# Kernel optimization log

Measured on AMD Instinct MI355X. Metric: run time of the kernel, lower is better.

The kernel has to match this reference:

```python
import jax, jax.numpy as jnp
import numpy as np

GRID = 104          # grid cells per side (832px input, stride 8)
NB = 9              # anchors per cell
NC = 80             # classes
INPUT_SIZE = 832    # draw canvas size
DET_T = 0.02        # detection threshold
NMS_T = 0.3         # IoU threshold
MAX_BOXES = 50      # per-class NMS cap
N = GRID * GRID * NB


def setup_inputs() -> dict:
    key = jax.random.key(0)
    k1, k2 = jax.random.split(key)
    inputs = jax.random.normal(k1, (1, GRID, GRID, NB, 5 + NC), dtype=jnp.float32)
    anchors = jax.random.uniform(k2, (NB, 2), dtype=jnp.float32, minval=0.5, maxval=GRID / 2.0)
    return {"inputs": inputs, "anchors": anchors}


def _iou_one_vs_all(box, boxes):
    # box [4], boxes [N,4]; coordinate order is irrelevant to IoU as long as consistent
    x1 = jnp.maximum(box[0], boxes[:, 0]); y1 = jnp.maximum(box[1], boxes[:, 1])
    x2 = jnp.minimum(box[2], boxes[:, 2]); y2 = jnp.minimum(box[3], boxes[:, 3])
    inter = jnp.maximum(x2 - x1, 0.0) * jnp.maximum(y2 - y1, 0.0)
    a0 = (box[2] - box[0]) * (box[3] - box[1])
    a1 = (boxes[:, 2] - boxes[:, 0]) * (boxes[:, 3] - boxes[:, 1])
    union = a0 + a1 - inter
    return jnp.where(union > 0, inter / union, 0.0)


def _forward(inputs, anchors):
    # ---- decode boxes ----
    gy, gx = jnp.meshgrid(jnp.arange(GRID), jnp.arange(GRID), indexing='ij')
    c_grid = jnp.stack([gx, gy], axis=-1).astype(inputs.dtype)[None, :, :, None, :]  # (1,G,G,1,2)
    b_xy = (jax.nn.sigmoid(inputs[..., 0:2]) + c_grid) / GRID
    b_wh = jnp.exp(inputs[..., 2:4]) * anchors[None, None, None, :, :] / GRID
    boxes = jnp.concatenate([b_xy - b_wh / 2.0, b_xy + b_wh / 2.0], axis=-1)
    scores_all = jax.nn.sigmoid(inputs[..., 4:5]) * jax.nn.softmax(inputs[..., 5:], axis=-1)
    scores_all = scores_all * (scores_all > DET_T).astype(scores_all.dtype)
    classes = jnp.argmax(scores_all, axis=-1)
    scores = jnp.max(scores_all, axis=-1)

    fboxes = boxes.reshape(N, 4)
    fscores = scores.reshape(N)
    fclasses = classes.reshape(N)

    # ---- per-class masked scores [NC, N] ----
    cls_mask = (fclasses[None, :] == jnp.arange(NC)[:, None]) & (fscores[None, :] > 0)
    cls_scores = jnp.where(cls_mask, fscores[None, :], 0.0)

    # ---- greedy NMS, vmapped over classes ----
    def nms_one(s):
        def body(i, carry):
            s, inds, valid = carry
            idx = jnp.argmax(s)
            v = s[idx] > 0
            ious = _iou_one_vs_all(fboxes[idx], fboxes)
            s = jnp.where(ious > NMS_T, 0.0, s).at[idx].set(0.0)
            return s, inds.at[i].set(idx), valid.at[i].set(v)
        init = (s, jnp.zeros(MAX_BOXES, jnp.int32), jnp.zeros(MAX_BOXES, dtype=bool))
        _, inds, valid = jax.lax.fori_loop(0, MAX_BOXES, body, init)
        return inds, valid

    inds, valid = jax.vmap(nms_one)(cls_scores)  # [NC, MAX_BOXES]
    sel = inds.reshape(-1)
    val = valid.reshape(-1)
    sboxes = fboxes[sel]  # [NC*MAX_BOXES, 4]; TF interprets as (y1, x1, y2, x2)

    # ---- draw bounding boxes on (1,H,W,1) canvas ----
    H = W = INPUT_SIZE
    def to_px(v, size):
        return jnp.clip(jnp.round(v * (size - 1)), 0, size - 1).astype(jnp.int32)
    r1 = to_px(sboxes[:, 0], H); c1 = to_px(sboxes[:, 1], W)
    r2 = to_px(sboxes[:, 2], H); c2 = to_px(sboxes[:, 3], W)
    cols = jnp.arange(W); rows = jnp.arange(H)
    col_in = ((cols[None, :] >= c1[:, None]) & (cols[None, :] <= c2[:, None]) & val[:, None]).astype(jnp.float32)
    row_in = ((rows[None, :] >= r1[:, None]) & (rows[None, :] <= r2[:, None]) & val[:, None]).astype(jnp.float32)
    canvas = jnp.zeros((H, W), jnp.float32)
    canvas = canvas.at[r1].add(col_in).at[r2].add(col_in)          # horizontal edges
    canvas = (canvas.T.at[c1].add(row_in).at[c2].add(row_in)).T   # vertical edges
    return (canvas > 0).astype(jnp.float32)[None, :, :, None]


def reference(inputs, anchors):
    return _forward(inputs, anchors)
```

## Files before the change

### kernel.cpp

```cpp
#pragma clang fp contract(off)
#include <hip/hip_runtime.h>
#include <math.h>

#define G       104
#define NBA     9
#define NC      80
#define NBOX    (G*G*NBA)
#define CH      (5+NC)
#define DET_T_  0.02f
#define NMS_T_  0.3f
#define MAXB    50
#define SORTN   2048
#define IMG     832
#define DB      128

typedef unsigned long long u64;
typedef unsigned int       u32;

__device__ __forceinline__ float sigmoidf_(float x) { return 1.0f / (1.0f + expf(-x)); }

__global__ __launch_bounds__(DB) void decode_kernel(const float* __restrict__ in,
        const float* __restrict__ anchors,
        float4* __restrict__ boxById, u64* __restrict__ allKey, float4* __restrict__ out4)
{
    __shared__ float lds[DB * CH];
    const int tid = threadIdx.x;

    {
        const int CZ = (IMG*IMG/4 + 760) / 761;
        int zbase = blockIdx.x * CZ;
        for (int i = tid; i < CZ; i += DB) {
            int idx = zbase + i;
            if (idx < IMG*IMG/4) out4[idx] = make_float4(0, 0, 0, 0);
        }
    }

    const int base = blockIdx.x * (DB * CH);
    int nfl = NBOX * CH - base;
    if (nfl > DB * CH) nfl = DB * CH;

    int nv4 = nfl >> 2;
    const float4* gin4 = (const float4*)(in + base);
    for (int i = tid; i < nv4; i += DB) ((float4*)lds)[i] = gin4[i];
    for (int i = (nv4 << 2) + tid; i < nfl; i += DB) lds[i] = in[base + i];
    __syncthreads();

    int n = blockIdx.x * DB + tid;
    if (n >= NBOX) return;
    const float* p = lds + tid * CH;

    float v[CH];
#pragma unroll
    for (int k = 0; k < CH; ++k) v[k] = p[k];

    float m = v[5];
#pragma unroll
    for (int i = 1; i < NC; ++i) m = fmaxf(m, v[5 + i]);

    float sum = 0.0f;
    u64 cm0 = 0, cm1 = 0;
#pragma unroll
    for (int i = 0; i < NC; ++i) {
        float d = v[5 + i] - m;
        sum += expf(d);
        u64 cand = (d >= -2.0e-6f) ? 1ull : 0ull;
        if (i < 64) cm0 |= cand << i;
        else        cm1 |= cand << (i - 64);
    }
    float obj = sigmoidf_(v[4]);

    float best = -1.0f; int bcls = 0;
    while (cm0) {
        int i = __ffsll((long long)cm0) - 1; cm0 &= cm0 - 1;
        float e = expf(p[5 + i] - m);
        float s = obj * (e / sum);
        if (s > best) { best = s; bcls = i; }
    }
    while (cm1) {
        int i = __ffsll((long long)cm1) - 1 + 64; cm1 &= cm1 - 1;
        float e = expf(p[5 + i] - m);
        float s = obj * (e / sum);
        if (s > best) { best = s; bcls = i; }
    }

    u64 key = 0;
    if (best > DET_T_) {
        int a  = n % NBA;
        int t2 = n / NBA;
        int gx = t2 % G;
        int gy = t2 / G;
        float bx = (sigmoidf_(v[0]) + (float)gx) / (float)G;
        float by = (sigmoidf_(v[1]) + (float)gy) / (float)G;
        float bw = expf(v[2]) * anchors[2*a + 0] / (float)G;
        float bh = expf(v[3]) * anchors[2*a + 1] / (float)G;
        boxById[n] = make_float4(bx - bw / 2.0f, by - bh / 2.0f,
                                 bx + bw / 2.0f, by + bh / 2.0f);
        key = ((u64)__float_as_uint(best) << 24) | ((u64)(131071 - n) << 7) | (u64)bcls;
    }
    allKey[n] = key;
}

__device__ __forceinline__ int to_px(float v) {
    float r = rintf(v * 831.0f);
    r = fminf(fmaxf(r, 0.0f), 831.0f);
    return (int)r;
}

__device__ __forceinline__ bool iou_gt_pre(const float4 W, float aW,
                                           const float4 C, float aC) {
    float x1 = fmaxf(W.x, C.x), y1 = fmaxf(W.y, C.y);
    float x2 = fminf(W.z, C.z), y2 = fminf(W.w, C.w);
    float inter = fmaxf(x2 - x1, 0.0f) * fmaxf(y2 - y1, 0.0f);
    float uni = aW + aC - inter;
    float iou = (uni > 0.0f) ? (inter / uni) : 0.0f;
    return iou > NMS_T_;
}

__device__ __forceinline__ u64 cex_shfl(u64 r, int x, int stride, int size) {
    u64 v = __shfl_xor(r, stride);
    bool asc   = (x & size) != 0;
    bool upper = (x & stride) != 0;
    bool keep_max = (!asc) != upper;
    u64 mx = (r > v) ? r : v;
    u64 mn = (r > v) ? v : r;
    return keep_max ? mx : mn;
}

__global__ __launch_bounds__(1024) void nms_draw_kernel(
    const float4* __restrict__ boxById, const u64* __restrict__ allKey,
    float* __restrict__ out)
{
    __shared__ u64    skey[SORTN];
    __shared__ float4 sbox[SORTN];
    __shared__ float4 selb[MAXB];
    __shared__ float  swa[MAXB];
    __shared__ u64    csA[16], csB[16], sfirst[16];
    __shared__ int    s_nsel, s_bad, s_cnt;

    const int c = blockIdx.x;
    const int t = threadIdx.x;
    const int w = t >> 6, l = t & 63;
    const int eA = (w << 7) + l, eB = eA + 64;

    if (t == 0) { s_bad = 0; s_nsel = 0; s_cnt = 0; }
    for (int i = t; i < SORTN; i += 1024) skey[i] = 0;
    __syncthreads();

    {
        const ulonglong2* ak2 = (const ulonglong2*)allKey;
        for (int pi = t; pi < NBOX/2; pi += 1024) {
            ulonglong2 kk = ak2[pi];
            if (kk.x != 0ull && (int)(kk.x & 0x7F) == c) {
                int pos = atomicAdd(&s_cnt, 1);
                if (pos < SORTN) skey[pos] = kk.x;
            }
            if (kk.y != 0ull && (int)(kk.y & 0x7F) == c) {
                int pos = atomicAdd(&s_cnt, 1);
                if (pos < SORTN) skey[pos] = kk.y;
            }
        }
    }
    __syncthreads();
    int count = s_cnt; if (count > SORTN) count = SORTN;

    u64 rA = skey[eA];
    u64 rB = skey[eB];

    {
        u64 x = rA ^ rB;
#pragma unroll
        for (int off = 32; off >= 1; off >>= 1) x ^= __shfl_xor(x, off);
        if (l == 0) csA[w] = x;
    }

#pragma unroll
    for (int size = 2; size <= 64; size <<= 1)
        for (int stride = size >> 1; stride >= 1; stride >>= 1) {
            rA = cex_shfl(rA, eA, stride, size);
            rB = cex_shfl(rB, eB, stride, size);
        }
    {
        const int size = 128;
        bool asc = (eA & 128) != 0;
        u64 mx = (rA > rB) ? rA : rB, mn = (rA > rB) ? rB : rA;
        rA = asc ? mn : mx; rB = asc ? mx : mn;
        for (int stride = 32; stride >= 1; stride >>= 1) {
            rA = cex_shfl(rA, eA, stride, size);
            rB = cex_shfl(rB, eB, stride, size);
        }
    }

    for (int size = 256; size <= 2048; size <<= 1) {
        skey[eA] = rA; skey[eB] = rB;
        __syncthreads();
        for (int stride = size >> 1; stride >= 128; stride >>= 1) {
            int i = ((t & ~(stride - 1)) << 1) | (t & (stride - 1));
            int j = i | stride;
            bool asc = (i & size) != 0;
            u64 ki = skey[i], kj = skey[j];
            bool sw = asc ? (ki > kj) : (ki < kj);
            if (sw) { skey[i] = kj; skey[j] = ki; }
            __syncthreads();
        }
        rA = skey[eA]; rB = skey[eB];
        bool asc = (eA & size) != 0;
        u64 mx = (rA > rB) ? rA : rB, mn = (rA > rB) ? rB : rA;
        rA = asc ? mn : mx; rB = asc ? mx : mn;
        for (int stride = 32; stride >= 1; stride >>= 1) {
            rA = cex_shfl(rA, eA, stride, size);
            rB = cex_shfl(rB, eB, stride, size);
        }
    }

    {
        u64 x = rA ^ rB;
#pragma unroll
        for (int off = 32; off >= 1; off >>= 1) x ^= __shfl_xor(x, off);
        if (l == 0) { csB[w] = x; sfirst[w] = rA; }
        bool bad = false;
        u64 dA  = __shfl_down(rA, 1);
        u64 dB  = __shfl_down(rB, 1);
        u64 rB0 = __shfl(rB, 0);
        if (l < 63) { bad |= (rA < dA); bad |= (rB < dB); }
        if (l == 63) bad |= (rA < rB0);
        __syncthreads();
        if (l == 63 && w < 15) bad |= (rB < sfirst[w + 1]);
        if (t == 0) {
            u64 X0 = 0, X1 = 0;
            for (int i = 0; i < 16; ++i) { X0 ^= csA[i]; X1 ^= csB[i]; }
            if (X0 != X1) s_bad = 1;
        }
        if (bad) s_bad = 1;
        __syncthreads();
    }

    if (s_bad) {
        for (int i = t; i < SORTN; i += 1024) skey[i] = 0;
        if (t == 0) s_cnt = 0;
        __syncthreads();
        for (int i = t; i < NBOX; i += 1024) {
            u64 k = allKey[i];
            if (k != 0ull && (int)(k & 0x7F) == c) {
                int pos = atomicAdd(&s_cnt, 1);
                if (pos < SORTN) skey[pos] = k;
            }
        }
        __syncthreads();
        for (int ph = 0; ph < SORTN; ++ph) {
            int i = (t << 1) + (ph & 1);
            if (i + 1 < SORTN) {
                u64 a = skey[i], b = skey[i + 1];
                if (a < b) { skey[i] = b; skey[i + 1] = a; }
            }
            __syncthreads();
        }
        rA = skey[eA]; rB = skey[eB];
    }

    if (eA < count) sbox[eA] = boxById[131071 - (int)((rA >> 7) & 0x1FFFF)];
    if (eB < count) sbox[eB] = boxById[131071 - (int)((rB >> 7) & 0x1FFFF)];
    __syncthreads();

    if (t < 64) {
        const int lane = t;
        int nsel = 0;
        for (int p0 = 0; p0 < count && nsel < MAXB; p0 += 64) {
            int p = p0 + lane;
            bool have = (p < count);
            float4 C = sbox[have ? p : 0];
            float aC = (C.z - C.x) * (C.w - C.y);

            bool sup = false;
#pragma unroll 4
            for (int ww = 0; ww < nsel; ++ww)
                sup |= iou_gt_pre(selb[ww], swa[ww], C, aC);

            u64 alive = __ballot(have && !sup);
            while (alive != 0ull && nsel < MAXB) {
                int i = __ffsll((long long)alive) - 1;
                float4 Wn = make_float4(__shfl(C.x, i), __shfl(C.y, i),
                                        __shfl(C.z, i), __shfl(C.w, i));
                float aWn = __shfl(aC, i);
                if (lane == 0) { selb[nsel] = Wn; swa[nsel] = aWn; }
                ++nsel;
                u64 killed = __ballot(have && iou_gt_pre(Wn, aWn, C, aC));
                alive &= ~killed;
            }
        }
        if (lane == 0) s_nsel = nsel;
    }
    __syncthreads();

    int nsel = s_nsel;
    int lane = t & 63;
    for (int b = t >> 6; b < nsel; b += 16) {
        float4 B = selb[b];
        int r1 = to_px(B.x), c1 = to_px(B.y), r2 = to_px(B.z), c2 = to_px(B.w);
        for (int i = c1 + lane; i <= c2; i += 64) {
            out[r1*IMG + i] = 1.0f;
            out[r2*IMG + i] = 1.0f;
        }
        for (int i = r1 + lane; i <= r2; i += 64) {
            out[i*IMG + c1] = 1.0f;
            out[i*IMG + c2] = 1.0f;
        }
    }
}

extern "C" void kernel_launch(void* const* d_in, const int* in_sizes, int n_in,
                              void* d_out, int out_size, void* d_ws, size_t ws_size,
                              hipStream_t stream)
{
    const float* in      = (const float*)d_in[0];
    const float* anchors = (const float*)d_in[1];
    float* out           = (float*)d_out;

    char* ws = (char*)d_ws;
    float4* boxById = (float4*)ws;
    u64*    allKey  = (u64*)(ws + (size_t)NBOX * sizeof(float4));

    decode_kernel<<<(NBOX + DB - 1)/DB, DB, 0, stream>>>(in, anchors, boxById, allKey,
                                                         (float4*)out);
    nms_draw_kernel<<<NC, 1024, 0, stream>>>(boxById, allKey, out);
}
```

Before: 79.70 us.

## Split drawing into row-tiled kernel with LDS canvas instead of scattered global writes

Removes the canvas zeroing from the decode kernel and the scattered global stores from the NMS kernel. NMS now writes the selected boxes as pixel coordinates to a workspace buffer. A new draw kernel gives each block 8 image rows, rasterises every selected box into an LDS row buffer with a run queue for horizontal edges, and writes the rows out coalesced. This trades one extra kernel launch and a full scan of all 4000 box slots per block for no separate zero pass and no uncoalesced global writes.

```diff
diff --git a/kernel.cpp b/kernel.cpp
--- a/kernel.cpp
+++ b/kernel.cpp
@@ -10,9 +10,13 @@
 #define DET_T_  0.02f
 #define NMS_T_  0.3f
 #define MAXB    50
+#define NSEL    (NC*MAXB)
 #define SORTN   2048
 #define IMG     832
 #define DB      128
+#define RPB     8
+#define DCHUNK  1024
+#define RQCAP   (2*DCHUNK)
 
 typedef unsigned long long u64;
 typedef unsigned int       u32;
@@ -21,19 +25,10 @@
 
 __global__ __launch_bounds__(DB) void decode_kernel(const float* __restrict__ in,
         const float* __restrict__ anchors,
-        float4* __restrict__ boxById, u64* __restrict__ allKey, float4* __restrict__ out4)
+        float4* __restrict__ boxById, u64* __restrict__ allKey)
 {
     __shared__ float lds[DB * CH];
     const int tid = threadIdx.x;
-
-    {
-        const int CZ = (IMG*IMG/4 + 760) / 761;
-        int zbase = blockIdx.x * CZ;
-        for (int i = tid; i < CZ; i += DB) {
-            int idx = zbase + i;
-            if (idx < IMG*IMG/4) out4[idx] = make_float4(0, 0, 0, 0);
-        }
-    }
 
     const int base = blockIdx.x * (DB * CH);
     int nfl = NBOX * CH - base;
@@ -126,9 +121,9 @@
     return keep_max ? mx : mn;
 }
 
-__global__ __launch_bounds__(1024) void nms_draw_kernel(
+__global__ __launch_bounds__(1024) void nms_select_kernel(
     const float4* __restrict__ boxById, const u64* __restrict__ allKey,
-    float* __restrict__ out)
+    ushort4* __restrict__ selPx)
 {
     __shared__ u64    skey[SORTN];
     __shared__ float4 sbox[SORTN];
@@ -292,19 +287,67 @@
     __syncthreads();
 
     int nsel = s_nsel;
-    int lane = t & 63;
-    for (int b = t >> 6; b < nsel; b += 16) {
-        float4 B = selb[b];
-        int r1 = to_px(B.x), c1 = to_px(B.y), r2 = to_px(B.z), c2 = to_px(B.w);
-        for (int i = c1 + lane; i <= c2; i += 64) {
-            out[r1*IMG + i] = 1.0f;
-            out[r2*IMG + i] = 1.0f;
-        }
-        for (int i = r1 + lane; i <= r2; i += 64) {
-            out[i*IMG + c1] = 1.0f;
-            out[i*IMG + c2] = 1.0f;
-        }
-    }
+    for (int k = t; k < MAXB; k += 1024) {
+        ushort4 px = make_ushort4(0xFFFF, 0xFFFF, 0xFFFF, 0xFFFF);
+        if (k < nsel) {
+            float4 B = selb[k];
+            px = make_ushort4((unsigned short)to_px(B.x), (unsigned short)to_px(B.y),
+                              (unsigned short)to_px(B.z), (unsigned short)to_px(B.w));
+        }
+        selPx[c*MAXB + k] = px;
+    }
+}
+
+__global__ __launch_bounds__(256) void draw_rows_kernel(const ushort4* __restrict__ selPx,
+                                                        float* __restrict__ out)
+{
+    __shared__ float   row[RPB * IMG];
+    __shared__ ushort4 runq[RQCAP];
+    __shared__ int     s_nrun;
+
+    const int t  = threadIdx.x;
+    const int wv = t >> 6, ln = t & 63;
+    const int r0 = blockIdx.x * RPB;
+
+    for (int i = t; i < RPB * IMG; i += 256) row[i] = 0.0f;
+    __syncthreads();
+
+    for (int cb = 0; cb < NSEL; cb += DCHUNK) {
+        if (t == 0) s_nrun = 0;
+        __syncthreads();
+
+        int cend = cb + DCHUNK; if (cend > NSEL) cend = NSEL;
+        for (int b = cb + t; b < cend; b += 256) {
+            ushort4 B = selPx[b];
+            if (B.x == 0xFFFF) continue;
+            int r1 = B.x, c1 = B.y, r2 = B.z, c2 = B.w;
+#pragma unroll
+            for (int rl = 0; rl < RPB; ++rl) {
+                int r = r0 + rl;
+                if (r >= r1 && r <= r2) {
+                    row[rl*IMG + c1] = 1.0f;
+                    row[rl*IMG + c2] = 1.0f;
+                    if (r == r1 || r == r2) {
+                        int qi = atomicAdd(&s_nrun, 1);
+                        runq[qi] = make_ushort4((unsigned short)rl, B.y, B.w, 0);
+                    }
+                }
+            }
+        }
+        __syncthreads();
+
+        int nrun = s_nrun;
+        for (int q = wv; q < nrun; q += 4) {
+            ushort4 R = runq[q];
+            int base = (int)R.x * IMG;
+            for (int i = (int)R.y + ln; i <= (int)R.z; i += 64) row[base + i] = 1.0f;
+        }
+        __syncthreads();
+    }
+
+    float4* o4 = (float4*)(out + r0 * IMG);
+    for (int i = t; i < RPB * IMG / 4; i += 256)
+        o4[i] = make_float4(row[4*i], row[4*i+1], row[4*i+2], row[4*i+3]);
 }
 
 extern "C" void kernel_launch(void* const* d_in, const int* in_sizes, int n_in,
@@ -316,10 +359,11 @@
     float* out           = (float*)d_out;
 
     char* ws = (char*)d_ws;
-    float4* boxById = (float4*)ws;
-    u64*    allKey  = (u64*)(ws + (size_t)NBOX * sizeof(float4));
-
-    decode_kernel<<<(NBOX + DB - 1)/DB, DB, 0, stream>>>(in, anchors, boxById, allKey,
-                                                         (float4*)out);
-    nms_draw_kernel<<<NC, 1024, 0, stream>>>(boxById, allKey, out);
-}
+    float4*  boxById = (float4*)ws;
+    u64*     allKey  = (u64*)(ws + (size_t)NBOX * sizeof(float4));
+    ushort4* selPx   = (ushort4*)(ws + (size_t)NBOX * (sizeof(float4) + sizeof(u64)));
+
+    decode_kernel<<<(NBOX + DB - 1)/DB, DB, 0, stream>>>(in, anchors, boxById, allKey);
+    nms_select_kernel<<<NC, 1024, 0, stream>>>(boxById, allKey, selPx);
+    draw_rows_kernel<<<(IMG + RPB - 1)/RPB, 256, 0, stream>>>(selPx, out);
+}
```

Result: slower. 104.2 us (+30.7%).
